# Performance work log

Measured on AMD Instinct MI355X. Metric: run time of the kernel, lower is better.

## Reference

```python
import jax, jax.numpy as jnp
import numpy as np

MIN_VAL = 0.0
MAX_VAL = 1.0
NUM_BINS = 512
NUM_NODES = 128
GRAD_SMOOTH = 0.01
BIN_W = (MAX_VAL - MIN_VAL) / NUM_BINS


def _make_kernels():
    sobel = jnp.array([-1.0, 0.0, 1.0], dtype=jnp.float32) / (2.0 * BIN_W)
    r = max(1, int(GRAD_SMOOTH / BIN_W))  # kernel radius in bins
    idx = jnp.arange(2 * r + 1, dtype=jnp.float32) - r
    sigma = GRAD_SMOOTH / BIN_W
    g = jnp.exp(-0.5 * (idx / sigma) ** 2)
    return sobel, g / jnp.sum(g)


def _conv1d_reflect(x, k):
    # x: [N, B], k: [K]; torch Conv1d = cross-correlation with reflect padding
    pad = (k.shape[0] - 1) // 2
    xp = jnp.pad(x, ((0, 0), (pad, pad)), mode='reflect')
    out = jax.lax.conv_general_dilated(
        xp[:, None, :], k[None, None, :], (1,), 'VALID',
        dimension_numbers=('NCH', 'OIH', 'NCH'))
    return out[:, 0, :]


def _compute_cdf_pdf(residuals, weights, src_indices, dst_indices):
    # histogram bin per sample (floor)
    bi = jnp.floor((residuals - MIN_VAL) / BIN_W).astype(jnp.int32)
    valid = (bi >= 0) & (bi < NUM_BINS)
    bi = jnp.clip(bi, 0, NUM_BINS - 1)
    wc = (weights * valid).reshape(-1)  # [N_pairs*K]

    src_comb = (src_indices[:, None] * NUM_BINS + bi).reshape(-1)
    dst_comb = (dst_indices[:, None] * NUM_BINS + bi).reshape(-1)
    nseg = NUM_NODES * NUM_BINS
    hist = (jax.ops.segment_sum(wc, src_comb, num_segments=nseg)
            + jax.ops.segment_sum(wc, dst_comb, num_segments=nseg))
    hist = hist.reshape(NUM_NODES, NUM_BINS)

    wflat = weights.reshape(-1)
    src_exp = jnp.broadcast_to(src_indices[:, None], residuals.shape).reshape(-1)
    dst_exp = jnp.broadcast_to(dst_indices[:, None], residuals.shape).reshape(-1)
    tw = (jax.ops.segment_sum(wflat, src_exp, num_segments=NUM_NODES)
          + jax.ops.segment_sum(wflat, dst_exp, num_segments=NUM_NODES))

    pmf = hist / (tw[:, None] + 1e-10)
    cdf = jnp.cumsum(pmf, axis=1)
    sobel, gauss = _make_kernels()
    pdf = _conv1d_reflect(_conv1d_reflect(cdf, sobel), gauss)
    return cdf, pdf


def _lookup(residuals, weights, cdf, pdf, src_indices, dst_indices):
    # rounded bin for lookup (floor of x + 0.5)
    bi = jnp.floor((residuals - MIN_VAL) / BIN_W + 0.5).astype(jnp.int32)
    valid = (bi >= 0) & (bi < NUM_BINS) & (weights > 0.0)
    bi = jnp.clip(bi, 0, NUM_BINS - 1)
    src_cdf = cdf[src_indices[:, None], bi]
    dst_cdf = cdf[dst_indices[:, None], bi]
    src_grad = pdf[src_indices[:, None], bi] * weights
    dst_grad = pdf[dst_indices[:, None], bi] * weights
    two = jnp.float32(2.0)
    return (jnp.where(valid, src_cdf, two),
            jnp.where(valid, src_grad, 0.0),
            jnp.where(valid, dst_cdf, two),
            jnp.where(valid, dst_grad, 0.0))


def setup_inputs() -> dict:
    key = jax.random.key(0)
    k1, k2, k3, k4 = jax.random.split(key, 4)
    N_pairs, K = 1024, 16384
    return {
        'residuals': jax.random.uniform(k1, (N_pairs, K), dtype=jnp.float32),
        'weights': jax.random.uniform(k2, (N_pairs, K), dtype=jnp.float32),
        'src_indices': jax.random.randint(k3, (N_pairs,), 0, NUM_NODES),
        'dst_indices': jax.random.randint(k4, (N_pairs,), 0, NUM_NODES),
    }


def reference(residuals, weights, src_indices, dst_indices):
    cdf, pdf = _compute_cdf_pdf(residuals, weights, src_indices, dst_indices)
    src_cdf, _, dst_cdf, _ = _lookup(residuals, weights, cdf, pdf,
                                     src_indices, dst_indices)
    return src_cdf, dst_cdf
```

## Files before the change

### kernel.cpp

```cpp
#include <hip/hip_runtime.h>

#define NUM_BINS  512
#define NUM_NODES 128
#define K_ELEMS   16384
#define N_PAIRS   1024
#define NCOPY     32

__device__ __forceinline__ void gfadd(float* p, float v) { unsafeAtomicAdd(p, v); }

__global__ __launch_bounds__(256) void zero_ws_kernel(float* __restrict__ ws, int n)
{
    int i = blockIdx.x * 256 + threadIdx.x;
    if (i < n) ws[i] = 0.0f;
}

__global__ __launch_bounds__(512) void hist_kernel(
    const float* __restrict__ residuals, const float* __restrict__ weights,
    const int* __restrict__ src, const int* __restrict__ dst,
    float* __restrict__ hist, float* __restrict__ tw)
{
    __shared__ unsigned lh[NUM_BINS * NCOPY];
    __shared__ float swsum[8];
    const int row  = blockIdx.x;
    const int t    = threadIdx.x;
    const int copy = t & 31;

    uint4* lh4 = (uint4*)lh;
    #pragma unroll
    for (int k = 0; k < NUM_BINS * NCOPY / 4 / 512; ++k) {
        uint4 z; z.x = z.y = z.z = z.w = 0u;
        lh4[t + k * 512] = z;
    }
    __syncthreads();

    const float4* r4 = (const float4*)(residuals + (size_t)row * K_ELEMS);
    const float4* w4 = (const float4*)(weights   + (size_t)row * K_ELEMS);

    float wsum = 0.0f;
    #pragma unroll
    for (int it = 0; it < K_ELEMS / 4 / 512; ++it) {
        float4 r = r4[t + it * 512];
        float4 w = w4[t + it * 512];
        wsum += w.x + w.y + w.z + w.w;

        int b;
        b = (int)floorf(r.x * 512.0f);
        if ((unsigned)b < 512u) atomicAdd(&lh[b * NCOPY + copy], (unsigned)fmaf(w.x, 65536.0f, 0.5f));
        b = (int)floorf(r.y * 512.0f);
        if ((unsigned)b < 512u) atomicAdd(&lh[b * NCOPY + copy], (unsigned)fmaf(w.y, 65536.0f, 0.5f));
        b = (int)floorf(r.z * 512.0f);
        if ((unsigned)b < 512u) atomicAdd(&lh[b * NCOPY + copy], (unsigned)fmaf(w.z, 65536.0f, 0.5f));
        b = (int)floorf(r.w * 512.0f);
        if ((unsigned)b < 512u) atomicAdd(&lh[b * NCOPY + copy], (unsigned)fmaf(w.w, 65536.0f, 0.5f));
    }

    #pragma unroll
    for (int off = 32; off > 0; off >>= 1) wsum += __shfl_down(wsum, off, 64);
    const int wave = t >> 6, lane = t & 63;
    if (lane == 0) swsum[wave] = wsum;
    __syncthreads();

    const int s = src[row], d = dst[row];
    if (t == 0) {
        float tot = 0.0f;
        #pragma unroll
        for (int i = 0; i < 8; ++i) tot += swsum[i];
        gfadd(&tw[s], tot);
        gfadd(&tw[d], tot);
    }

    {
        float tot = 0.0f;
        #pragma unroll
        for (int cc = 0; cc < NCOPY; ++cc)
            tot += (float)lh[t * NCOPY + ((t + cc) & 31)];
        tot *= (1.0f / 65536.0f);
        gfadd(&hist[s * NUM_BINS + t], tot);
        gfadd(&hist[d * NUM_BINS + t], tot);
    }
}

__global__ __launch_bounds__(512) void scan_kernel(float* __restrict__ hist,
                                                   const float* __restrict__ tw)
{
    __shared__ float s[NUM_BINS];
    const int node = blockIdx.x;
    const int t    = threadIdx.x;

    const float denom = tw[node] + 1e-10f;
    s[t] = hist[node * NUM_BINS + t] / denom;
    __syncthreads();

    for (int off = 1; off < NUM_BINS; off <<= 1) {
        float add = (t >= off) ? s[t - off] : 0.0f;
        __syncthreads();
        s[t] += add;
        __syncthreads();
    }
    hist[node * NUM_BINS + t] = s[t];
}

__global__ __launch_bounds__(256) void lookup_kernel(
    const float* __restrict__ residuals, const float* __restrict__ weights,
    const int* __restrict__ src, const int* __restrict__ dst,
    const float* __restrict__ cdf,
    float* __restrict__ out_src, float* __restrict__ out_dst)
{
    __shared__ float scdf[NUM_BINS];
    __shared__ float dcdf[NUM_BINS];
    const int CHUNK = K_ELEMS / 4;
    const int row   = blockIdx.x >> 2;
    const int chunk = blockIdx.x & 3;
    const int t     = threadIdx.x;

    const int s = src[row], d = dst[row];
    for (int i = t; i < NUM_BINS; i += 256) {
        scdf[i] = cdf[s * NUM_BINS + i];
        dcdf[i] = cdf[d * NUM_BINS + i];
    }
    __syncthreads();

    const size_t base = (size_t)row * K_ELEMS + (size_t)chunk * CHUNK;
    const float4* r4  = (const float4*)(residuals + base);
    const float4* w4  = (const float4*)(weights   + base);
    float4*       os4 = (float4*)(out_src + base);
    float4*       od4 = (float4*)(out_dst + base);

    for (int i = t; i < CHUNK / 4; i += 256) {
        float4 r = r4[i], w = w4[i];
        float4 osv, odv;

        {   int b = (int)floorf(r.x * 512.0f + 0.5f);
            bool valid = (b >= 0) & (b < NUM_BINS) & (w.x > 0.0f);
            int bc = min(max(b, 0), NUM_BINS - 1);
            osv.x = valid ? scdf[bc] : 2.0f;
            odv.x = valid ? dcdf[bc] : 2.0f; }
        {   int b = (int)floorf(r.y * 512.0f + 0.5f);
            bool valid = (b >= 0) & (b < NUM_BINS) & (w.y > 0.0f);
            int bc = min(max(b, 0), NUM_BINS - 1);
            osv.y = valid ? scdf[bc] : 2.0f;
            odv.y = valid ? dcdf[bc] : 2.0f; }
        {   int b = (int)floorf(r.z * 512.0f + 0.5f);
            bool valid = (b >= 0) & (b < NUM_BINS) & (w.z > 0.0f);
            int bc = min(max(b, 0), NUM_BINS - 1);
            osv.z = valid ? scdf[bc] : 2.0f;
            odv.z = valid ? dcdf[bc] : 2.0f; }
        {   int b = (int)floorf(r.w * 512.0f + 0.5f);
            bool valid = (b >= 0) & (b < NUM_BINS) & (w.w > 0.0f);
            int bc = min(max(b, 0), NUM_BINS - 1);
            osv.w = valid ? scdf[bc] : 2.0f;
            odv.w = valid ? dcdf[bc] : 2.0f; }

        os4[i] = osv;
        od4[i] = odv;
    }
}

extern "C" void kernel_launch(void* const* d_in, const int* in_sizes, int n_in,
                              void* d_out, int out_size, void* d_ws, size_t ws_size,
                              hipStream_t stream)
{
    const float* residuals = (const float*)d_in[0];
    const float* weights   = (const float*)d_in[1];
    const int*   src       = (const int*)d_in[2];
    const int*   dst       = (const int*)d_in[3];

    float* out_src = (float*)d_out;
    float* out_dst = out_src + (size_t)N_PAIRS * K_ELEMS;

    float* hist = (float*)d_ws;
    float* tw   = hist + NUM_NODES * NUM_BINS;

    const int ws_elems = NUM_NODES * NUM_BINS + NUM_NODES;
    zero_ws_kernel<<<(ws_elems + 255) / 256, 256, 0, stream>>>((float*)d_ws, ws_elems);

    hist_kernel<<<N_PAIRS, 512, 0, stream>>>(residuals, weights, src, dst, hist, tw);

    scan_kernel<<<NUM_NODES, NUM_BINS, 0, stream>>>(hist, tw);

    lookup_kernel<<<N_PAIRS * 4, 256, 0, stream>>>(residuals, weights, src, dst,
                                                   hist, out_src, out_dst);
}
```

Measured before the change: 78.76 us.

## Precompute lookup bin codes in histogram pass to shrink lookup reads

```diff
diff --git a/kernel.cpp b/kernel.cpp
--- a/kernel.cpp
+++ b/kernel.cpp
@@ -14,22 +14,24 @@
     if (i < n) ws[i] = 0.0f;
 }
 
-__global__ __launch_bounds__(512) void hist_kernel(
+template<bool WRITE_CODES>
+__global__ __launch_bounds__(1024) void hist_kernel(
     const float* __restrict__ residuals, const float* __restrict__ weights,
     const int* __restrict__ src, const int* __restrict__ dst,
-    float* __restrict__ hist, float* __restrict__ tw)
+    float* __restrict__ hist, float* __restrict__ tw,
+    unsigned short* __restrict__ codes)
 {
     __shared__ unsigned lh[NUM_BINS * NCOPY];
-    __shared__ float swsum[8];
+    __shared__ float swsum[16];
     const int row  = blockIdx.x;
     const int t    = threadIdx.x;
     const int copy = t & 31;
 
     uint4* lh4 = (uint4*)lh;
     #pragma unroll
-    for (int k = 0; k < NUM_BINS * NCOPY / 4 / 512; ++k) {
+    for (int k = 0; k < NUM_BINS * NCOPY / 4 / 1024; ++k) {
         uint4 z; z.x = z.y = z.z = z.w = 0u;
-        lh4[t + k * 512] = z;
+        lh4[t + k * 1024] = z;
     }
     __syncthreads();
 
@@ -38,9 +40,9 @@
 
     float wsum = 0.0f;
     #pragma unroll
-    for (int it = 0; it < K_ELEMS / 4 / 512; ++it) {
-        float4 r = r4[t + it * 512];
-        float4 w = w4[t + it * 512];
+    for (int it = 0; it < K_ELEMS / 4 / 1024; ++it) {
+        float4 r = r4[t + it * 1024];
+        float4 w = w4[t + it * 1024];
         wsum += w.x + w.y + w.z + w.w;
 
         int b;
@@ -52,6 +54,20 @@
         if ((unsigned)b < 512u) atomicAdd(&lh[b * NCOPY + copy], (unsigned)fmaf(w.z, 65536.0f, 0.5f));
         b = (int)floorf(r.w * 512.0f);
         if ((unsigned)b < 512u) atomicAdd(&lh[b * NCOPY + copy], (unsigned)fmaf(w.w, 65536.0f, 0.5f));
+
+        if (WRITE_CODES) {
+            ushort4 c;
+            int lb;
+            lb = (int)floorf(r.x * 512.0f + 0.5f);
+            c.x = (unsigned short)((((unsigned)lb < 512u) & (w.x > 0.0f)) ? lb : 0xFFFF);
+            lb = (int)floorf(r.y * 512.0f + 0.5f);
+            c.y = (unsigned short)((((unsigned)lb < 512u) & (w.y > 0.0f)) ? lb : 0xFFFF);
+            lb = (int)floorf(r.z * 512.0f + 0.5f);
+            c.z = (unsigned short)((((unsigned)lb < 512u) & (w.z > 0.0f)) ? lb : 0xFFFF);
+            lb = (int)floorf(r.w * 512.0f + 0.5f);
+            c.w = (unsigned short)((((unsigned)lb < 512u) & (w.w > 0.0f)) ? lb : 0xFFFF);
+            ((ushort4*)(codes + (size_t)row * K_ELEMS))[t + it * 1024] = c;
+        }
     }
 
     #pragma unroll
@@ -64,19 +80,24 @@
     if (t == 0) {
         float tot = 0.0f;
         #pragma unroll
-        for (int i = 0; i < 8; ++i) tot += swsum[i];
+        for (int i = 0; i < 16; ++i) tot += swsum[i];
         gfadd(&tw[s], tot);
         gfadd(&tw[d], tot);
     }
 
     {
+        const int bin  = t >> 1;
+        const int half = t & 1;
         float tot = 0.0f;
         #pragma unroll
-        for (int cc = 0; cc < NCOPY; ++cc)
-            tot += (float)lh[t * NCOPY + ((t + cc) & 31)];
+        for (int cc = 0; cc < 16; ++cc) {
+            const int c2 = (((bin + cc) & 15) | (half << 4));
+            tot += (float)lh[bin * NCOPY + c2];
+        }
+        tot += __shfl_xor(tot, 1);
         tot *= (1.0f / 65536.0f);
-        gfadd(&hist[s * NUM_BINS + t], tot);
-        gfadd(&hist[d * NUM_BINS + t], tot);
+        if (half == 0) gfadd(&hist[s * NUM_BINS + bin], tot);
+        else           gfadd(&hist[d * NUM_BINS + bin], tot);
     }
 }
 
@@ -100,8 +121,8 @@
     hist[node * NUM_BINS + t] = s[t];
 }
 
-__global__ __launch_bounds__(256) void lookup_kernel(
-    const float* __restrict__ residuals, const float* __restrict__ weights,
+__global__ __launch_bounds__(256) void lookup_code_kernel(
+    const unsigned short* __restrict__ codes,
     const int* __restrict__ src, const int* __restrict__ dst,
     const float* __restrict__ cdf,
     float* __restrict__ out_src, float* __restrict__ out_dst)
@@ -121,6 +142,47 @@
     __syncthreads();
 
     const size_t base = (size_t)row * K_ELEMS + (size_t)chunk * CHUNK;
+    const ushort4* c4 = (const ushort4*)(codes + base);
+    float4*       os4 = (float4*)(out_src + base);
+    float4*       od4 = (float4*)(out_dst + base);
+
+    for (int i = t; i < CHUNK / 4; i += 256) {
+        ushort4 c = c4[i];
+        float4 osv, odv;
+        osv.x = (c.x != 0xFFFF) ? scdf[c.x] : 2.0f;
+        odv.x = (c.x != 0xFFFF) ? dcdf[c.x] : 2.0f;
+        osv.y = (c.y != 0xFFFF) ? scdf[c.y] : 2.0f;
+        odv.y = (c.y != 0xFFFF) ? dcdf[c.y] : 2.0f;
+        osv.z = (c.z != 0xFFFF) ? scdf[c.z] : 2.0f;
+        odv.z = (c.z != 0xFFFF) ? dcdf[c.z] : 2.0f;
+        osv.w = (c.w != 0xFFFF) ? scdf[c.w] : 2.0f;
+        odv.w = (c.w != 0xFFFF) ? dcdf[c.w] : 2.0f;
+        os4[i] = osv;
+        od4[i] = odv;
+    }
+}
+
+__global__ __launch_bounds__(256) void lookup_kernel(
+    const float* __restrict__ residuals, const float* __restrict__ weights,
+    const int* __restrict__ src, const int* __restrict__ dst,
+    const float* __restrict__ cdf,
+    float* __restrict__ out_src, float* __restrict__ out_dst)
+{
+    __shared__ float scdf[NUM_BINS];
+    __shared__ float dcdf[NUM_BINS];
+    const int CHUNK = K_ELEMS / 4;
+    const int row   = blockIdx.x >> 2;
+    const int chunk = blockIdx.x & 3;
+    const int t     = threadIdx.x;
+
+    const int s = src[row], d = dst[row];
+    for (int i = t; i < NUM_BINS; i += 256) {
+        scdf[i] = cdf[s * NUM_BINS + i];
+        dcdf[i] = cdf[d * NUM_BINS + i];
+    }
+    __syncthreads();
+
+    const size_t base = (size_t)row * K_ELEMS + (size_t)chunk * CHUNK;
     const float4* r4  = (const float4*)(residuals + base);
     const float4* w4  = (const float4*)(weights   + base);
     float4*       os4 = (float4*)(out_src + base);
@@ -129,7 +191,6 @@
     for (int i = t; i < CHUNK / 4; i += 256) {
         float4 r = r4[i], w = w4[i];
         float4 osv, odv;
-
         {   int b = (int)floorf(r.x * 512.0f + 0.5f);
             bool valid = (b >= 0) & (b < NUM_BINS) & (w.x > 0.0f);
             int bc = min(max(b, 0), NUM_BINS - 1);
@@ -150,7 +211,6 @@
             int bc = min(max(b, 0), NUM_BINS - 1);
             osv.w = valid ? scdf[bc] : 2.0f;
             odv.w = valid ? dcdf[bc] : 2.0f; }
-
         os4[i] = osv;
         od4[i] = odv;
     }
@@ -171,13 +231,30 @@
     float* hist = (float*)d_ws;
     float* tw   = hist + NUM_NODES * NUM_BINS;
 
+    const size_t hist_bytes  = (size_t)(NUM_NODES * NUM_BINS + NUM_NODES) * 4;
+    const size_t codes_off   = 262656;
+    const size_t codes_bytes = (size_t)N_PAIRS * K_ELEMS * 2;
+    const bool   use_codes   = ws_size >= codes_off + codes_bytes;
+    unsigned short* codes = (unsigned short*)((char*)d_ws + codes_off);
+
     const int ws_elems = NUM_NODES * NUM_BINS + NUM_NODES;
     zero_ws_kernel<<<(ws_elems + 255) / 256, 256, 0, stream>>>((float*)d_ws, ws_elems);
 
-    hist_kernel<<<N_PAIRS, 512, 0, stream>>>(residuals, weights, src, dst, hist, tw);
+    if (use_codes) {
+        hist_kernel<true><<<N_PAIRS, 1024, 0, stream>>>(residuals, weights, src, dst,
+                                                        hist, tw, codes);
+    } else {
+        hist_kernel<false><<<N_PAIRS, 1024, 0, stream>>>(residuals, weights, src, dst,
+                                                         hist, tw, codes);
+    }
 
     scan_kernel<<<NUM_NODES, NUM_BINS, 0, stream>>>(hist, tw);
 
-    lookup_kernel<<<N_PAIRS * 4, 256, 0, stream>>>(residuals, weights, src, dst,
-                                                   hist, out_src, out_dst);
-}
+    if (use_codes) {
+        lookup_code_kernel<<<N_PAIRS * 4, 256, 0, stream>>>(codes, src, dst,
+                                                            hist, out_src, out_dst);
+    } else {
+        lookup_kernel<<<N_PAIRS * 4, 256, 0, stream>>>(residuals, weights, src, dst,
+                                                       hist, out_src, out_dst);
+    }
+}
```

Result: faster. 74.53 us (-5.4%).
